# Kernel optimization log

Measured on AMD Instinct MI355X. Metric: run time of the kernel, lower is better.

Reference implementation:

```python
import jax, jax.numpy as jnp
import numpy as np

G = 64          # groups of the dynamic conv
EPS = 1e-5      # instance-norm epsilon


def setup_inputs() -> dict:
    key = jax.random.key(0)
    ks = jax.random.split(key, 12)
    B, Cin, Cout, S = 16, 512, 256, 512   # batch, in_ch, out_ch, style_dim
    H = W = 32
    cg = Cin // G                          # channels per group (= 8)

    def n(k, shape, scale=0.05):
        return jax.random.normal(k, shape, dtype=jnp.float32) * scale

    return {
        "x": jax.random.normal(ks[0], (B, Cin, H, W), dtype=jnp.float32),
        "w": jax.random.normal(ks[1], (B, S, 3, 3), dtype=jnp.float32),
        # KernelPredictor params
        "kp_sw": n(ks[2], (Cin * cg, S, 3, 3)),   # spatial (depthwise) kernel predictor conv
        "kp_sb": n(ks[3], (Cin * cg,)),
        "kp_pw": n(ks[4], (Cin * cg, S)),          # pointwise kernel predictor (1x1 on pooled style)
        "kp_pb": n(ks[5], (Cin * cg,)),
        "kp_bw": n(ks[6], (Cin, S)),               # bias predictor
        "kp_bb": n(ks[7], (Cin,)),
        # decoder conv stack (convs=2, last changes channels)
        "dec_w1": n(ks[8], (Cin, Cin, 3, 3)),
        "dec_b1": n(ks[9], (Cin,)),
        "dec_w2": n(ks[10], (Cout, Cin, 3, 3)),
        "dec_b2": n(ks[11], (Cout,)),
    }


def _conv(x, w, b=None, groups=1, pad=((1, 1), (1, 1))):
    y = jax.lax.conv_general_dilated(
        x, w, (1, 1), pad, feature_group_count=groups,
        dimension_numbers=("NCHW", "OIHW", "NCHW"))
    if b is not None:
        y = y + b[None, :, None, None]
    return y


def _instance_norm(x):
    m = x.mean(axis=(2, 3), keepdims=True)
    v = x.var(axis=(2, 3), keepdims=True)
    return (x - m) * jax.lax.rsqrt(v + EPS)


def reference(x, w, kp_sw, kp_sb, kp_pw, kp_pb, kp_bw, kp_bb,
              dec_w1, dec_b1, dec_w2, dec_b2):
    B, C, H, W_ = x.shape
    cg = C // G
    # ---- KernelPredictor ----
    # spatial branch: reflect-padded 3x3 conv over the 3x3 style map -> per-sample grouped spatial kernels
    w_pad = jnp.pad(w, ((0, 0), (0, 0), (1, 1), (1, 1)), mode="reflect")
    dw = _conv(w_pad, kp_sw, kp_sb, pad=((0, 0), (0, 0)))      # [B, C*cg, 3, 3]
    dw = dw.reshape(B, C, cg, 3, 3)                             # [B, out, in/g, kh, kw]
    # pointwise + bias branches: global avg pool then 1x1 conv (== matmul)
    pooled = w.mean(axis=(2, 3))                                # [B, S]
    pw = (pooled @ kp_pw.T + kp_pb).reshape(B, G, cg, cg)       # [B, g, out_pg, in_pg]
    bias = pooled @ kp_bw.T + kp_bb                             # [B, C]
    # ---- AdaConv2D: instance-norm, per-sample grouped spatial conv, grouped pointwise conv + bias ----
    xn = _instance_norm(x)
    xp = jnp.pad(xn, ((0, 0), (0, 0), (1, 1), (1, 1)), mode="reflect")

    def per_sample(xi, ki):
        return _conv(xi[None], ki, groups=G, pad=((0, 0), (0, 0)))[0]

    y = jax.vmap(per_sample)(xp, dw)                            # [B, C, H, W]
    yg = y.reshape(B, G, cg, H, W_)
    y = jnp.einsum("bgoi,bgihw->bgohw", pw, yg).reshape(B, C, H, W_)
    y = y + bias[:, :, None, None]
    # ---- decoder conv stack + nearest upsample ----
    y = jax.nn.relu(_conv(y, dec_w1, dec_b1))
    y = jax.nn.relu(_conv(y, dec_w2, dec_b2))
    y = jnp.repeat(jnp.repeat(y, 2, axis=2), 2, axis=3)         # 32x32 -> 64x64 nearest
    return y
```

## Files before the change

### kernel.cpp

```cpp
#include <hip/hip_runtime.h>

using short8 = __attribute__((ext_vector_type(8))) short;
using f32x4  = __attribute__((ext_vector_type(4))) float;

__device__ __forceinline__ unsigned short f2b(float f){
  unsigned int u = __float_as_uint(f);
  u = u + 0x7fffu + ((u >> 16) & 1u);
  return (unsigned short)(u >> 16);
}
__device__ __forceinline__ float b2f(unsigned short s){
  return __uint_as_float(((unsigned int)s) << 16);
}

__device__ __forceinline__ void gll16(const void* g, void* l){
  __builtin_amdgcn_global_load_lds(
      (const __attribute__((address_space(1))) unsigned int*)g,
      (__attribute__((address_space(3))) unsigned int*)l, 16, 0, 0);
}
__device__ __forceinline__ void vm_wait4(){ asm volatile("s_waitcnt vmcnt(4)" ::: "memory"); }
__device__ __forceinline__ void vm_wait0(){ asm volatile("s_waitcnt vmcnt(0)" ::: "memory"); }

__global__ __launch_bounds__(256) void k_prepwt(const float* __restrict__ w,
    unsigned short* __restrict__ A, float* __restrict__ pooled,
    const float* __restrict__ w1, const float* __restrict__ w2,
    unsigned short* __restrict__ d1, unsigned short* __restrict__ d2){
  int bid = blockIdx.x;
  if(bid >= 176){
    __shared__ float ld[4608];
    int co = bid - 176;
    const float* src = (co < 512) ? (w1 + (size_t)co * 4608) : (w2 + (size_t)(co - 512) * 4608);
    unsigned short* dst = (co < 512) ? (d1 + (size_t)co * 4608) : (d2 + (size_t)(co - 512) * 4608);
    for(int i = threadIdx.x; i < 4608; i += 256) ld[i] = src[i];
    __syncthreads();
    for(int i = threadIdx.x; i < 4608; i += 256){
      int q = i >> 9, cin = i & 511;
      dst[i] = f2b(ld[cin * 9 + q]);
    }
    return;
  }
  if(bid >= 144){
    int i = (bid - 144) * 256 + threadIdx.x;
    const float* p = w + (size_t)i * 9;
    float s = 0.f;
    #pragma unroll
    for(int j = 0; j < 9; j++) s += p[j];
    pooled[i] = s * (1.f / 9.f);
    return;
  }
  int row = bid;
  int pos = row >> 4, b = row & 15;
  int oh = pos / 3, ow = pos % 3;
  for(int k = threadIdx.x; k < 4608; k += 256){
    int cin = k / 9, q = k - cin * 9;
    int kh = q / 3, kw = q - kh * 3;
    int ih = oh + kh - 1, iw = ow + kw - 1;
    ih = ih < 0 ? -ih : (ih > 2 ? 4 - ih : ih);
    iw = iw < 0 ? -iw : (iw > 2 ? 4 - iw : iw);
    float v = w[((size_t)(b * 512 + cin) * 3 + ih) * 3 + iw];
    A[(size_t)row * 4608 + k] = f2b(v);
  }
}

__global__ __launch_bounds__(256) void k_pwbias(const float* __restrict__ pooled,
    const float* __restrict__ kp_pw, const float* __restrict__ kp_pb,
    const float* __restrict__ kp_bw, const float* __restrict__ kp_bb,
    float* __restrict__ pw, float* __restrict__ bias){
  int wid = (blockIdx.x * 256 + threadIdx.x) >> 6;
  int lane = threadIdx.x & 63;
  const float* row;
  float bv;
  if(wid < 4096){ row = kp_pw + (size_t)wid * 512; bv = kp_pb[wid]; }
  else          { row = kp_bw + (size_t)(wid - 4096) * 512; bv = kp_bb[wid - 4096]; }
  float r[8];
  #pragma unroll
  for(int i = 0; i < 8; i++) r[i] = row[lane + 64 * i];
  for(int b = 0; b < 16; b++){
    float s = 0.f;
    #pragma unroll
    for(int i = 0; i < 8; i++) s += r[i] * pooled[b * 512 + lane + 64 * i];
    #pragma unroll
    for(int o = 32; o >= 1; o >>= 1) s += __shfl_xor(s, o, 64);
    if(lane == 0){
      if(wid < 4096) pw[b * 4096 + wid] = s + bv;
      else           bias[b * 512 + (wid - 4096)] = s + bv;
    }
  }
}

__global__ __launch_bounds__(256) void k_gemmB(const unsigned short* __restrict__ Aim,
    const float* __restrict__ kp_sw, float* __restrict__ part){
  __shared__ unsigned short Al[144 * 72];
  __shared__ unsigned short Bl[64 * 72];
  int tid = threadIdx.x;
  int lane = tid & 63, wv = tid >> 6;
  int n0 = blockIdx.x * 64;
  int kz = blockIdx.y;
  f32x4 acc[9] = {};
  for(int ks = kz * 6; ks < kz * 6 + 6; ks++){
    int kb = ks * 64;
    for(int c = tid; c < 1152; c += 256){
      int m = c >> 3, kc = c & 7;
      *(int4*)&Al[m * 72 + kc * 8] = *(const int4*)(Aim + (size_t)m * 4608 + kb + kc * 8);
    }
    for(int c = tid; c < 512; c += 256){
      int n = c >> 3, kc = c & 7;
      const float4* src = (const float4*)(kp_sw + (size_t)(n0 + n) * 4608 + kb + kc * 8);
      float4 v0 = src[0], v1 = src[1];
      unsigned short tmp[8];
      tmp[0]=f2b(v0.x); tmp[1]=f2b(v0.y); tmp[2]=f2b(v0.z); tmp[3]=f2b(v0.w);
      tmp[4]=f2b(v1.x); tmp[5]=f2b(v1.y); tmp[6]=f2b(v1.z); tmp[7]=f2b(v1.w);
      *(int4*)&Bl[n * 72 + kc * 8] = *(int4*)tmp;
    }
    __syncthreads();
    int r16 = lane & 15, khalf = lane >> 4;
    #pragma unroll
    for(int kk = 0; kk < 2; kk++){
      int ko = kk * 32 + khalf * 8;
      short8 bf = *(const short8*)&Bl[(wv * 16 + r16) * 72 + ko];
      #pragma unroll
      for(int mf = 0; mf < 9; mf++){
        short8 af = *(const short8*)&Al[(mf * 16 + r16) * 72 + ko];
        acc[mf] = __builtin_amdgcn_mfma_f32_16x16x32_bf16(af, bf, acc[mf], 0, 0, 0);
      }
    }
    __syncthreads();
  }
  int r16 = lane & 15, rgrp = lane >> 4;
  int n = n0 + wv * 16 + r16;
  #pragma unroll
  for(int mf = 0; mf < 9; mf++){
    #pragma unroll
    for(int r = 0; r < 4; r++){
      int m = mf * 16 + rgrp * 4 + r;
      part[((size_t)kz * 144 + m) * 4096 + n] = acc[mf][r];
    }
  }
}

__global__ __launch_bounds__(256) void k_red(const float* __restrict__ part,
    const float* __restrict__ kp_sb, float* __restrict__ dw){
  int i = blockIdx.x * 256 + threadIdx.x;
  int m = i >> 12, n = i & 4095;
  float s = kp_sb[n];
  #pragma unroll
  for(int kz = 0; kz < 12; kz++) s += part[((size_t)kz * 144 + m) * 4096 + n];
  int q = m >> 4, b = m & 15;
  dw[((size_t)b * 4096 + n) * 9 + q] = s;
}

__global__ __launch_bounds__(256) void k_ada(const float* __restrict__ x,
    const float* __restrict__ dwb, const float* __restrict__ pwb,
    const float* __restrict__ biasb, unsigned short* __restrict__ y0p,
    unsigned short* __restrict__ y1p){
  int bg = blockIdx.x;
  if(bg >= 1024){
    int i = (bg - 1024) * 256 + threadIdx.x;
    int b = i / 8448, rem = i - b * 8448;
    int e = rem >> 6, ch8 = rem & 63;
    int hh, ww;
    if(e < 34){ hh = 0; ww = e; }
    else if(e < 68){ hh = 33; ww = e - 34; }
    else if(e < 100){ hh = e - 68 + 1; ww = 0; }
    else { hh = e - 100 + 1; ww = 33; }
    int4 z = {0, 0, 0, 0};
    *(int4*)&y1p[((size_t)(b * 34 + hh) * 34 + ww) * 512 + ch8 * 8] = z;
    return;
  }
  __shared__ float xn[8][1156];
  __shared__ float dwl[576];
  __shared__ float pwl[64];
  __shared__ float bl[8];
  __shared__ float red0[4][8], red1[4][8];
  __shared__ float ms[8], rs[8];
  int b = bg >> 6, g = bg & 63;
  int tid = threadIdx.x;
  int lane = tid & 63, wv = tid >> 6;
  for(int i = tid; i < 576; i += 256) dwl[i] = dwb[((size_t)b * 4096 + g * 64) * 9 + i];
  if(tid < 64) pwl[tid] = pwb[b * 4096 + g * 64 + tid];
  if(tid < 8)  bl[tid]  = biasb[b * 512 + g * 8 + tid];
  if(tid < 132){
    int e = tid, hh, ww;
    if(e < 34){ hh = 0; ww = e; }
    else if(e < 68){ hh = 33; ww = e - 34; }
    else if(e < 100){ hh = e - 68 + 1; ww = 0; }
    else { hh = e - 100 + 1; ww = 33; }
    int4 z = {0, 0, 0, 0};
    *(int4*)&y0p[((size_t)(b * 34 + hh) * 34 + ww) * 512 + g * 8] = z;
  }
  const float* xb = x + ((size_t)(b * 512 + g * 8)) * 1024;
  int h4 = tid >> 3, w4 = (tid & 7) * 4;
  float s[8], s2[8];
  #pragma unroll
  for(int ci = 0; ci < 8; ci++){
    float4 v = *(const float4*)(xb + ci * 1024 + tid * 4);
    float* dst = &xn[ci][(h4 + 1) * 34 + w4 + 1];
    dst[0] = v.x; dst[1] = v.y; dst[2] = v.z; dst[3] = v.w;
    s[ci]  = v.x + v.y + v.z + v.w;
    s2[ci] = v.x * v.x + v.y * v.y + v.z * v.z + v.w * v.w;
  }
  #pragma unroll
  for(int ci = 0; ci < 8; ci++){
    #pragma unroll
    for(int o = 32; o >= 1; o >>= 1){
      s[ci]  += __shfl_xor(s[ci],  o, 64);
      s2[ci] += __shfl_xor(s2[ci], o, 64);
    }
  }
  if(lane == 0){
    #pragma unroll
    for(int ci = 0; ci < 8; ci++){ red0[wv][ci] = s[ci]; red1[wv][ci] = s2[ci]; }
  }
  __syncthreads();
  if(tid < 8){
    float S  = red0[0][tid] + red0[1][tid] + red0[2][tid] + red0[3][tid];
    float S2 = red1[0][tid] + red1[1][tid] + red1[2][tid] + red1[3][tid];
    float m = S * (1.f / 1024.f);
    ms[tid] = m;
    rs[tid] = rsqrtf(S2 * (1.f / 1024.f) - m * m + 1e-5f);
  }
  __syncthreads();
  #pragma unroll
  for(int ci = 0; ci < 8; ci++){
    float m = ms[ci], r = rs[ci];
    float* p = &xn[ci][(h4 + 1) * 34 + w4 + 1];
    #pragma unroll
    for(int j = 0; j < 4; j++) p[j] = (p[j] - m) * r;
  }
  __syncthreads();
  for(int idx = tid; idx < 1056; idx += 256){
    int ci = idx / 132, e = idx - ci * 132;
    int hh, ww;
    if(e < 34){ hh = 0; ww = e; }
    else if(e < 68){ hh = 33; ww = e - 34; }
    else if(e < 100){ hh = e - 68 + 1; ww = 0; }
    else { hh = e - 100 + 1; ww = 33; }
    int h = hh - 1, w2 = ww - 1;
    h  = h  < 0 ? 1 : (h  > 31 ? 30 : h);
    w2 = w2 < 0 ? 1 : (w2 > 31 ? 30 : w2);
    xn[ci][hh * 34 + ww] = xn[ci][(h + 1) * 34 + (w2 + 1)];
  }
  __syncthreads();
  float acc[4][8] = {};
  #pragma unroll
  for(int i = 0; i < 8; i++){
    #pragma unroll
    for(int q = 0; q < 9; q++){
      int kh = q / 3, kw = q - kh * 3;
      float dvs[8];
      #pragma unroll
      for(int o = 0; o < 8; o++) dvs[o] = dwl[(o * 8 + i) * 9 + q];
      #pragma unroll
      for(int pp = 0; pp < 4; pp++){
        int p = pp * 256 + tid; int h = p >> 5, w = p & 31;
        float v = xn[i][(h + kh) * 34 + (w + kw)];
        #pragma unroll
        for(int o = 0; o < 8; o++) acc[pp][o] += v * dvs[o];
      }
    }
  }
  #pragma unroll
  for(int pp = 0; pp < 4; pp++){
    int p = pp * 256 + tid; int h = p >> 5, w = p & 31;
    unsigned short pack[8];
    #pragma unroll
    for(int o = 0; o < 8; o++){
      float sv = bl[o];
      #pragma unroll
      for(int i2 = 0; i2 < 8; i2++) sv += pwl[o * 8 + i2] * acc[pp][i2];
      pack[o] = f2b(sv);
    }
    *(int4*)&y0p[((size_t)(b * 34 + h + 1) * 34 + (w + 1)) * 512 + g * 8] = *(int4*)pack;
  }
}

template<int NCOUT, int OUT_PADDED>
__global__ __launch_bounds__(512) void k_conv(const unsigned short* __restrict__ inp,
    const unsigned short* __restrict__ wt, const float* __restrict__ bias,
    unsigned short* __restrict__ outp){
  __shared__ unsigned short Al[2][128 * 64];
  __shared__ unsigned short Bl[2][128 * 64];
  int tid = threadIdx.x;
  int mt = blockIdx.x;
  int n0 = blockIdx.y * 128;
  int b = mt >> 3, h0 = (mt & 7) * 4;
  int lane = tid & 63, wv = tid >> 6;
  int wm = (wv >> 2) * 64, wn = (wv & 3) * 32;
  f32x4 acc[4][2] = {};
  const size_t bbase = (size_t)b * 34 * 34 * 512;

  int kc = tid & 7;
  int m0 = tid >> 3, m1 = (tid + 512) >> 3;
  int colA0 = kc ^ (m0 & 7), colA1 = kc ^ (m1 & 7);
  int mh0 = m0 >> 5, mw0 = m0 & 31;
  int mh1 = m1 >> 5, mw1 = m1 & 31;
  int ldsO0 = (tid & ~63) * 8;
  int ldsO1 = ldsO0 + 512 * 8;
  const unsigned short* a0base = inp + bbase + colA0 * 8;
  const unsigned short* a1base = inp + bbase + colA1 * 8;
  const unsigned short* b0base = wt + (size_t)(n0 + m0) * 4608 + colA0 * 8;
  const unsigned short* b1base = wt + (size_t)(n0 + m1) * 4608 + colA1 * 8;
  int r16 = lane & 15, khalf = lane >> 4;

#define STAGE(T, BUF) { \
    int q_ = (T) >> 3, cb_ = ((T) & 7) * 64; \
    int kh_ = q_ / 3, kw_ = q_ - kh_ * 3; \
    gll16(a0base + (size_t)((h0 + mh0 + kh_) * 34 + mw0 + kw_) * 512 + cb_, &Al[BUF][ldsO0]); \
    gll16(a1base + (size_t)((h0 + mh1 + kh_) * 34 + mw1 + kw_) * 512 + cb_, &Al[BUF][ldsO1]); \
    gll16(b0base + (size_t)q_ * 512 + cb_, &Bl[BUF][ldsO0]); \
    gll16(b1base + (size_t)q_ * 512 + cb_, &Bl[BUF][ldsO1]); }

#define COMPUTE(BUF) { \
    const unsigned short* Ab = Al[BUF]; const unsigned short* Bb = Bl[BUF]; \
    { int sc8 = (khalf ^ (r16 & 7)) * 8; \
      short8 af[4], bf[2]; \
      _Pragma("unroll") for(int i = 0; i < 4; i++) af[i] = *(const short8*)&Ab[(wm + i * 16 + r16) * 64 + sc8]; \
      _Pragma("unroll") for(int i = 0; i < 2; i++) bf[i] = *(const short8*)&Bb[(wn + i * 16 + r16) * 64 + sc8]; \
      __builtin_amdgcn_s_setprio(1); \
      _Pragma("unroll") for(int mi = 0; mi < 4; mi++) \
        _Pragma("unroll") for(int ni = 0; ni < 2; ni++) \
          acc[mi][ni] = __builtin_amdgcn_mfma_f32_16x16x32_bf16(af[mi], bf[ni], acc[mi][ni], 0, 0, 0); \
      __builtin_amdgcn_s_setprio(0); } \
    { int sc8 = ((4 + khalf) ^ (r16 & 7)) * 8; \
      short8 af[4], bf[2]; \
      _Pragma("unroll") for(int i = 0; i < 4; i++) af[i] = *(const short8*)&Ab[(wm + i * 16 + r16) * 64 + sc8]; \
      _Pragma("unroll") for(int i = 0; i < 2; i++) bf[i] = *(const short8*)&Bb[(wn + i * 16 + r16) * 64 + sc8]; \
      __builtin_amdgcn_s_setprio(1); \
      _Pragma("unroll") for(int mi = 0; mi < 4; mi++) \
        _Pragma("unroll") for(int ni = 0; ni < 2; ni++) \
          acc[mi][ni] = __builtin_amdgcn_mfma_f32_16x16x32_bf16(af[mi], bf[ni], acc[mi][ni], 0, 0, 0); \
      __builtin_amdgcn_s_setprio(0); } }

  STAGE(0, 0)
  STAGE(1, 1)
  vm_wait4(); __builtin_amdgcn_s_barrier();
  for(int t = 0; t < 70; t += 2){
    COMPUTE(0)
    __builtin_amdgcn_s_barrier();
    STAGE(t + 2, 0)
    vm_wait4(); __builtin_amdgcn_s_barrier();
    COMPUTE(1)
    __builtin_amdgcn_s_barrier();
    STAGE(t + 3, 1)
    vm_wait4(); __builtin_amdgcn_s_barrier();
  }
  COMPUTE(0)
  vm_wait0(); __builtin_amdgcn_s_barrier();
  COMPUTE(1)
#undef STAGE
#undef COMPUTE

  int rgrp = lane >> 4;
  #pragma unroll
  for(int ni = 0; ni < 2; ni++){
    int n = n0 + wn + ni * 16 + r16;
    float bv = bias[n];
    #pragma unroll
    for(int mi = 0; mi < 4; mi++){
      #pragma unroll
      for(int r = 0; r < 4; r++){
        int row = wm + mi * 16 + rgrp * 4 + r;
        int h = h0 + (row >> 5), w = row & 31;
        float v = acc[mi][ni][r] + bv;
        v = v > 0.f ? v : 0.f;
        size_t oidx;
        if(OUT_PADDED) oidx = ((size_t)(b * 34 + h + 1) * 34 + (w + 1)) * 512 + n;
        else           oidx = ((size_t)(b * 32 + h) * 32 + w) * NCOUT + n;
        outp[oidx] = f2b(v);
      }
    }
  }
}

__global__ __launch_bounds__(256) void k_up(const unsigned short* __restrict__ y2,
                                            float* __restrict__ out){
  __shared__ unsigned short ld[32 * 258];
  int bh = blockIdx.x; int b = bh >> 5, h = bh & 31;
  int tid = threadIdx.x;
  const unsigned short* src = y2 + ((size_t)b * 1024 + h * 32) * 256;
  for(int c = tid; c < 1024; c += 256){
    int w = c >> 5, kc = c & 31;
    *(int4*)&ld[w * 258 + kc * 8] = *(const int4*)&src[w * 256 + kc * 8];
  }
  __syncthreads();
  int q = tid & 3, co0 = tid >> 2;
  for(int cc = 0; cc < 4; cc++){
    int co = cc * 64 + co0;
    size_t obase = ((size_t)(b * 256 + co) * 64 + h * 2) * 64 + q * 16;
    #pragma unroll
    for(int i = 0; i < 4; i++){
      float a  = b2f(ld[(q * 8 + i * 2) * 258 + co]);
      float b2 = b2f(ld[(q * 8 + i * 2 + 1) * 258 + co]);
      float4 v = make_float4(a, a, b2, b2);
      *(float4*)&out[obase + i * 4]      = v;
      *(float4*)&out[obase + 64 + i * 4] = v;
    }
  }
}

extern "C" void kernel_launch(void* const* d_in, const int* in_sizes, int n_in,
                              void* d_out, int out_size, void* d_ws, size_t ws_size,
                              hipStream_t stream){
  (void)in_sizes; (void)n_in; (void)out_size; (void)ws_size;
  const float* x      = (const float*)d_in[0];
  const float* w      = (const float*)d_in[1];
  const float* kp_sw  = (const float*)d_in[2];
  const float* kp_sb  = (const float*)d_in[3];
  const float* kp_pw  = (const float*)d_in[4];
  const float* kp_pb  = (const float*)d_in[5];
  const float* kp_bw  = (const float*)d_in[6];
  const float* kp_bb  = (const float*)d_in[7];
  const float* dec_w1 = (const float*)d_in[8];
  const float* dec_b1 = (const float*)d_in[9];
  const float* dec_w2 = (const float*)d_in[10];
  const float* dec_b2 = (const float*)d_in[11];
  char* ws = (char*)d_ws;
  float*          pooled = (float*)(ws);
  float*          pw     = (float*)(ws + 32768);
  float*          bias   = (float*)(ws + 294912);
  unsigned short* Aim    = (unsigned short*)(ws + 393216);
  float*          dw     = (float*)(ws + 1720320);
  unsigned short* w1t    = (unsigned short*)(ws + 4079616);
  unsigned short* w2t    = (unsigned short*)(ws + 8798208);
  unsigned short* y0p    = (unsigned short*)(ws + 11157504);
  unsigned short* y1p    = (unsigned short*)(ws + 30097408);
  unsigned short* y2     = (unsigned short*)(ws + 49037312);
  float*          part   = (float*)(ws + 11157504);

  k_prepwt<<<944,  256, 0, stream>>>(w, Aim, pooled, dec_w1, dec_w2, w1t, w2t);
  k_pwbias<<<1152, 256, 0, stream>>>(pooled, kp_pw, kp_pb, kp_bw, kp_bb, pw, bias);
  k_gemmB <<<dim3(64, 12), 256, 0, stream>>>(Aim, kp_sw, part);
  k_red   <<<2304, 256, 0, stream>>>(part, kp_sb, dw);
  k_ada   <<<1552, 256, 0, stream>>>(x, dw, pw, bias, y0p, y1p);
  k_conv<512, 1><<<dim3(128, 4), 512, 0, stream>>>(y0p, w1t, dec_b1, y1p);
  k_conv<256, 0><<<dim3(128, 2), 512, 0, stream>>>(y1p, w2t, dec_b2, y2);
  k_up    <<<512,  256, 0, stream>>>(y2, (float*)d_out);
}
```

Baseline: 250.7 us.

## Fuse upsample into conv epilogue, split-K warps in conv, merge pwbias with gemm

```diff
diff --git a/kernel.cpp b/kernel.cpp
--- a/kernel.cpp
+++ b/kernel.cpp
@@ -61,40 +61,41 @@
   }
 }
 
-__global__ __launch_bounds__(256) void k_pwbias(const float* __restrict__ pooled,
+__global__ __launch_bounds__(256) void k_pwgemm(const unsigned short* __restrict__ Aim,
+    const float* __restrict__ kp_sw, float* __restrict__ part,
+    const float* __restrict__ pooled,
     const float* __restrict__ kp_pw, const float* __restrict__ kp_pb,
     const float* __restrict__ kp_bw, const float* __restrict__ kp_bb,
     float* __restrict__ pw, float* __restrict__ bias){
-  int wid = (blockIdx.x * 256 + threadIdx.x) >> 6;
-  int lane = threadIdx.x & 63;
-  const float* row;
-  float bv;
-  if(wid < 4096){ row = kp_pw + (size_t)wid * 512; bv = kp_pb[wid]; }
-  else          { row = kp_bw + (size_t)(wid - 4096) * 512; bv = kp_bb[wid - 4096]; }
-  float r[8];
-  #pragma unroll
-  for(int i = 0; i < 8; i++) r[i] = row[lane + 64 * i];
-  for(int b = 0; b < 16; b++){
-    float s = 0.f;
-    #pragma unroll
-    for(int i = 0; i < 8; i++) s += r[i] * pooled[b * 512 + lane + 64 * i];
-    #pragma unroll
-    for(int o = 32; o >= 1; o >>= 1) s += __shfl_xor(s, o, 64);
-    if(lane == 0){
-      if(wid < 4096) pw[b * 4096 + wid] = s + bv;
-      else           bias[b * 512 + (wid - 4096)] = s + bv;
-    }
-  }
-}
-
-__global__ __launch_bounds__(256) void k_gemmB(const unsigned short* __restrict__ Aim,
-    const float* __restrict__ kp_sw, float* __restrict__ part){
   __shared__ unsigned short Al[144 * 72];
   __shared__ unsigned short Bl[64 * 72];
+  int bid = blockIdx.x;
   int tid = threadIdx.x;
   int lane = tid & 63, wv = tid >> 6;
-  int n0 = blockIdx.x * 64;
-  int kz = blockIdx.y;
+  if(bid >= 768){
+    int wid = ((bid - 768) * 256 + tid) >> 6;
+    const float* row;
+    float bv;
+    if(wid < 4096){ row = kp_pw + (size_t)wid * 512; bv = kp_pb[wid]; }
+    else          { row = kp_bw + (size_t)(wid - 4096) * 512; bv = kp_bb[wid - 4096]; }
+    float r[8];
+    #pragma unroll
+    for(int i = 0; i < 8; i++) r[i] = row[lane + 64 * i];
+    for(int b = 0; b < 16; b++){
+      float s = 0.f;
+      #pragma unroll
+      for(int i = 0; i < 8; i++) s += r[i] * pooled[b * 512 + lane + 64 * i];
+      #pragma unroll
+      for(int o = 32; o >= 1; o >>= 1) s += __shfl_xor(s, o, 64);
+      if(lane == 0){
+        if(wid < 4096) pw[b * 4096 + wid] = s + bv;
+        else           bias[b * 512 + (wid - 4096)] = s + bv;
+      }
+    }
+    return;
+  }
+  int n0 = (bid & 63) * 64;
+  int kz = bid >> 6;
   f32x4 acc[9] = {};
   for(int ks = kz * 6; ks < kz * 6 + 6; ks++){
     int kb = ks * 64;
@@ -273,19 +274,22 @@
   }
 }
 
-template<int NCOUT, int OUT_PADDED>
-__global__ __launch_bounds__(512) void k_conv(const unsigned short* __restrict__ inp,
+template<int FUSE_UP>
+__global__ __launch_bounds__(512, 4) void k_convP(const unsigned short* __restrict__ inp,
     const unsigned short* __restrict__ wt, const float* __restrict__ bias,
-    unsigned short* __restrict__ outp){
-  __shared__ unsigned short Al[2][128 * 64];
-  __shared__ unsigned short Bl[2][128 * 64];
+    unsigned short* __restrict__ outp, float* __restrict__ outf){
+  __shared__ __align__(16) char smraw[65536];
+  unsigned short (*Al)[128 * 64] = (unsigned short(*)[128 * 64])smraw;
+  unsigned short (*Bl)[128 * 64] = (unsigned short(*)[128 * 64])(smraw + 32768);
+  float* red = (float*)smraw;
   int tid = threadIdx.x;
   int mt = blockIdx.x;
   int n0 = blockIdx.y * 128;
   int b = mt >> 3, h0 = (mt & 7) * 4;
   int lane = tid & 63, wv = tid >> 6;
-  int wm = (wv >> 2) * 64, wn = (wv & 3) * 32;
-  f32x4 acc[4][2] = {};
+  int khv = wv >> 2, wsub = wv & 3;
+  int wm = (wsub >> 1) * 64, wn = (wsub & 1) * 64;
+  f32x4 acc[4][4] = {};
   const size_t bbase = (size_t)b * 34 * 34 * 512;
 
   int kc = tid & 7;
@@ -300,6 +304,7 @@
   const unsigned short* b0base = wt + (size_t)(n0 + m0) * 4608 + colA0 * 8;
   const unsigned short* b1base = wt + (size_t)(n0 + m1) * 4608 + colA1 * 8;
   int r16 = lane & 15, khalf = lane >> 4;
+  int sc8 = ((khv * 4 + khalf) ^ (r16 & 7)) * 8;
 
 #define STAGE(T, BUF) { \
     int q_ = (T) >> 3, cb_ = ((T) & 7) * 64; \
@@ -310,25 +315,14 @@
     gll16(b1base + (size_t)q_ * 512 + cb_, &Bl[BUF][ldsO1]); }
 
 #define COMPUTE(BUF) { \
-    const unsigned short* Ab = Al[BUF]; const unsigned short* Bb = Bl[BUF]; \
-    { int sc8 = (khalf ^ (r16 & 7)) * 8; \
-      short8 af[4], bf[2]; \
-      _Pragma("unroll") for(int i = 0; i < 4; i++) af[i] = *(const short8*)&Ab[(wm + i * 16 + r16) * 64 + sc8]; \
-      _Pragma("unroll") for(int i = 0; i < 2; i++) bf[i] = *(const short8*)&Bb[(wn + i * 16 + r16) * 64 + sc8]; \
-      __builtin_amdgcn_s_setprio(1); \
-      _Pragma("unroll") for(int mi = 0; mi < 4; mi++) \
-        _Pragma("unroll") for(int ni = 0; ni < 2; ni++) \
-          acc[mi][ni] = __builtin_amdgcn_mfma_f32_16x16x32_bf16(af[mi], bf[ni], acc[mi][ni], 0, 0, 0); \
-      __builtin_amdgcn_s_setprio(0); } \
-    { int sc8 = ((4 + khalf) ^ (r16 & 7)) * 8; \
-      short8 af[4], bf[2]; \
-      _Pragma("unroll") for(int i = 0; i < 4; i++) af[i] = *(const short8*)&Ab[(wm + i * 16 + r16) * 64 + sc8]; \
-      _Pragma("unroll") for(int i = 0; i < 2; i++) bf[i] = *(const short8*)&Bb[(wn + i * 16 + r16) * 64 + sc8]; \
-      __builtin_amdgcn_s_setprio(1); \
-      _Pragma("unroll") for(int mi = 0; mi < 4; mi++) \
-        _Pragma("unroll") for(int ni = 0; ni < 2; ni++) \
-          acc[mi][ni] = __builtin_amdgcn_mfma_f32_16x16x32_bf16(af[mi], bf[ni], acc[mi][ni], 0, 0, 0); \
-      __builtin_amdgcn_s_setprio(0); } }
+    short8 af[4], bf[4]; \
+    _Pragma("unroll") for(int i = 0; i < 4; i++) af[i] = *(const short8*)&Al[BUF][(wm + i * 16 + r16) * 64 + sc8]; \
+    _Pragma("unroll") for(int i = 0; i < 4; i++) bf[i] = *(const short8*)&Bl[BUF][(wn + i * 16 + r16) * 64 + sc8]; \
+    __builtin_amdgcn_s_setprio(1); \
+    _Pragma("unroll") for(int mi = 0; mi < 4; mi++) \
+      _Pragma("unroll") for(int ni = 0; ni < 4; ni++) \
+        acc[mi][ni] = __builtin_amdgcn_mfma_f32_16x16x32_bf16(af[mi], bf[ni], acc[mi][ni], 0, 0, 0); \
+    __builtin_amdgcn_s_setprio(0); }
 
   STAGE(0, 0)
   STAGE(1, 1)
@@ -349,50 +343,55 @@
 #undef STAGE
 #undef COMPUTE
 
-  int rgrp = lane >> 4;
-  #pragma unroll
-  for(int ni = 0; ni < 2; ni++){
-    int n = n0 + wn + ni * 16 + r16;
-    float bv = bias[n];
-    #pragma unroll
-    for(int mi = 0; mi < 4; mi++){
-      #pragma unroll
-      for(int r = 0; r < 4; r++){
-        int row = wm + mi * 16 + rgrp * 4 + r;
-        int h = h0 + (row >> 5), w = row & 31;
-        float v = acc[mi][ni][r] + bv;
-        v = v > 0.f ? v : 0.f;
-        size_t oidx;
-        if(OUT_PADDED) oidx = ((size_t)(b * 34 + h + 1) * 34 + (w + 1)) * 512 + n;
-        else           oidx = ((size_t)(b * 32 + h) * 32 + w) * NCOUT + n;
-        outp[oidx] = f2b(v);
+  __syncthreads();
+  if(khv == 1){
+    float* dst = red + wsub * 4096 + lane * 4;
+    #pragma unroll
+    for(int mi = 0; mi < 4; mi++)
+      #pragma unroll
+      for(int ni = 0; ni < 4; ni++)
+        *(f32x4*)(dst + (mi * 4 + ni) * 256) = acc[mi][ni];
+  }
+  __syncthreads();
+  if(khv == 0){
+    const float* src = red + wsub * 4096 + lane * 4;
+    #pragma unroll
+    for(int mi = 0; mi < 4; mi++)
+      #pragma unroll
+      for(int ni = 0; ni < 4; ni++)
+        acc[mi][ni] += *(const f32x4*)(src + (mi * 4 + ni) * 256);
+
+    int rgrp = lane >> 4;
+    #pragma unroll
+    for(int ni = 0; ni < 4; ni++){
+      int n = n0 + wn + ni * 16 + r16;
+      float bv = bias[n];
+      #pragma unroll
+      for(int mi = 0; mi < 4; mi++){
+        int row0 = wm + mi * 16 + rgrp * 4;
+        int h = h0 + (row0 >> 5), w0 = row0 & 31;
+        float v[4];
+        #pragma unroll
+        for(int r = 0; r < 4; r++){
+          float t = acc[mi][ni][r] + bv;
+          v[r] = t > 0.f ? t : 0.f;
+        }
+        if(FUSE_UP){
+          size_t base = ((size_t)(b * 256 + n) * 64 + 2 * h) * 64 + 2 * w0;
+          float4 f0 = make_float4(v[0], v[0], v[1], v[1]);
+          float4 f1 = make_float4(v[2], v[2], v[3], v[3]);
+          *(float4*)&outf[base]          = f0;
+          *(float4*)&outf[base + 4]      = f1;
+          *(float4*)&outf[base + 64]     = f0;
+          *(float4*)&outf[base + 64 + 4] = f1;
+        } else {
+          #pragma unroll
+          for(int r = 0; r < 4; r++){
+            int w = w0 + r;
+            outp[((size_t)(b * 34 + h + 1) * 34 + (w + 1)) * 512 + n] = f2b(v[r]);
+          }
+        }
       }
-    }
-  }
-}
-
-__global__ __launch_bounds__(256) void k_up(const unsigned short* __restrict__ y2,
-                                            float* __restrict__ out){
-  __shared__ unsigned short ld[32 * 258];
-  int bh = blockIdx.x; int b = bh >> 5, h = bh & 31;
-  int tid = threadIdx.x;
-  const unsigned short* src = y2 + ((size_t)b * 1024 + h * 32) * 256;
-  for(int c = tid; c < 1024; c += 256){
-    int w = c >> 5, kc = c & 31;
-    *(int4*)&ld[w * 258 + kc * 8] = *(const int4*)&src[w * 256 + kc * 8];
-  }
-  __syncthreads();
-  int q = tid & 3, co0 = tid >> 2;
-  for(int cc = 0; cc < 4; cc++){
-    int co = cc * 64 + co0;
-    size_t obase = ((size_t)(b * 256 + co) * 64 + h * 2) * 64 + q * 16;
-    #pragma unroll
-    for(int i = 0; i < 4; i++){
-      float a  = b2f(ld[(q * 8 + i * 2) * 258 + co]);
-      float b2 = b2f(ld[(q * 8 + i * 2 + 1) * 258 + co]);
-      float4 v = make_float4(a, a, b2, b2);
-      *(float4*)&out[obase + i * 4]      = v;
-      *(float4*)&out[obase + 64 + i * 4] = v;
     }
   }
 }
@@ -423,15 +422,13 @@
   unsigned short* w2t    = (unsigned short*)(ws + 8798208);
   unsigned short* y0p    = (unsigned short*)(ws + 11157504);
   unsigned short* y1p    = (unsigned short*)(ws + 30097408);
-  unsigned short* y2     = (unsigned short*)(ws + 49037312);
   float*          part   = (float*)(ws + 11157504);
 
   k_prepwt<<<944,  256, 0, stream>>>(w, Aim, pooled, dec_w1, dec_w2, w1t, w2t);
-  k_pwbias<<<1152, 256, 0, stream>>>(pooled, kp_pw, kp_pb, kp_bw, kp_bb, pw, bias);
-  k_gemmB <<<dim3(64, 12), 256, 0, stream>>>(Aim, kp_sw, part);
+  k_pwgemm<<<1920, 256, 0, stream>>>(Aim, kp_sw, part, pooled,
+                                     kp_pw, kp_pb, kp_bw, kp_bb, pw, bias);
   k_red   <<<2304, 256, 0, stream>>>(part, kp_sb, dw);
   k_ada   <<<1552, 256, 0, stream>>>(x, dw, pw, bias, y0p, y1p);
-  k_conv<512, 1><<<dim3(128, 4), 512, 0, stream>>>(y0p, w1t, dec_b1, y1p);
-  k_conv<256, 0><<<dim3(128, 2), 512, 0, stream>>>(y1p, w2t, dec_b2, y2);
-  k_up    <<<512,  256, 0, stream>>>(y2, (float*)d_out);
-}
+  k_convP<0><<<dim3(128, 4), 512, 0, stream>>>(y0p, w1t, dec_b1, y1p, nullptr);
+  k_convP<1><<<dim3(128, 2), 512, 0, stream>>>(y1p, w2t, dec_b2, nullptr, (float*)d_out);
+}
```

Measured after the change: 219.4 us. -12.5%, faster.
